# Performance work log

Measured on AMD Instinct MI355X. Metric: run time of the kernel, lower is better.

The kernel has to match this reference:

```python
import jax, jax.numpy as jnp
import numpy as np


def l2norm(t, eps=1e-12):
    # matches F.normalize(p=2, dim=-1): divide by norm clamped to eps
    n = jnp.linalg.norm(t, axis=-1, keepdims=True)
    return t / jnp.maximum(n, eps)


def setup_inputs() -> dict:
    key = jax.random.key(0)
    kx, ke = jax.random.split(key)
    B, N, D, C = 8, 1024, 256, 8192
    x = jax.random.normal(kx, (B, N, D), dtype=jnp.float32)
    # codebook initialized l2-normalized, as in __init__ (kmeans_init=False)
    embed = l2norm(jax.random.normal(ke, (1, C, D), dtype=jnp.float32))
    return {"x": x, "embed": embed}


def reference(x, embed):
    # x: [B, N, D]; ndim < 4 -> add codebook dim h=1
    xh = x[None]                                   # [1, B, N, D]
    h, b, n, d = xh.shape
    flat = l2norm(xh.reshape(h, b * n, d))         # [1, B*N, D]
    e = l2norm(embed)                              # [1, C, D]
    # cosine-similarity distances
    dist = jnp.einsum('hnd,hcd->hnc', flat, e)     # [1, B*N, C]
    # sample_codebook_temp == 0 -> plain argmax
    idx = jnp.argmax(dist, axis=-1).reshape(h, b, n)  # [1, B, N]
    # batched_embedding: gather UN-normalized codebook rows
    quantize = jax.vmap(lambda em, ix: em[ix])(embed, idx)  # [1, B, N, D]
    # needs_codebook_dim -> strip leading dim
    return quantize[0], idx[0]
```

## Files before the change

### kernel.cpp

```cpp
#include <hip/hip_runtime.h>
#include <math.h>

#define QROWS 8192
#define DDIM  256
#define CCNT  8192

typedef __attribute__((ext_vector_type(4))) float f32x4;
typedef __attribute__((ext_vector_type(8))) short bf16x8;

__device__ __forceinline__ unsigned short f2bf(float f) {
    unsigned u = __float_as_uint(f);
    u += 0x7fffu + ((u >> 16) & 1u);
    return (unsigned short)(u >> 16);
}
__device__ __forceinline__ unsigned u32max(unsigned a, unsigned b) { return a > b ? a : b; }
__device__ __forceinline__ unsigned u32min(unsigned a, unsigned b) { return a < b ? a : b; }

__device__ __forceinline__ unsigned key32(float v, unsigned enc) {
    return ((__float_as_uint(v) ^ 0x80000000u) & 0xFFFFFF00u) | enc;
}

__global__ void k_prep(const float* __restrict__ x, unsigned short* __restrict__ xb,
                       const float* __restrict__ e, unsigned short* __restrict__ eb) {
    const int bid = blockIdx.x;
    if (bid < 1024) {
        const int i = (bid * 256 + threadIdx.x) * 8;
        const float4 f0 = *reinterpret_cast<const float4*>(x + i);
        const float4 f1 = *reinterpret_cast<const float4*>(x + i + 4);
        uint4 o;
        o.x = f2bf(f0.x) | ((unsigned)f2bf(f0.y) << 16);
        o.y = f2bf(f0.z) | ((unsigned)f2bf(f0.w) << 16);
        o.z = f2bf(f1.x) | ((unsigned)f2bf(f1.y) << 16);
        o.w = f2bf(f1.z) | ((unsigned)f2bf(f1.w) << 16);
        *reinterpret_cast<uint4*>(xb + i) = o;
    } else {
        const int row  = (bid - 1024) * 4 + (threadIdx.x >> 6);
        const int lane = threadIdx.x & 63;
        const float4 v = *reinterpret_cast<const float4*>(e + (size_t)row * DDIM + lane * 4);
        float s = v.x * v.x + v.y * v.y + v.z * v.z + v.w * v.w;
        #pragma unroll
        for (int off = 1; off < 64; off <<= 1) s += __shfl_xor(s, off);
        const float inv = 1.0f / fmaxf(sqrtf(s), 1e-12f);
        ushort4 o;
        o.x = f2bf(v.x * inv); o.y = f2bf(v.y * inv);
        o.z = f2bf(v.z * inv); o.w = f2bf(v.w * inv);
        *reinterpret_cast<ushort4*>(eb + (size_t)row * DDIM + lane * 4) = o;
    }
}

#define GLOAD_LDS(g, s) \
    __builtin_amdgcn_global_load_lds((const __attribute__((address_space(1))) void*)(g), \
                                     (__attribute__((address_space(3))) void*)(s), 16, 0, 0)

#define SBAR do { asm volatile("" ::: "memory"); __builtin_amdgcn_s_barrier(); \
                  asm volatile("" ::: "memory"); } while (0)
#define WAIT_LGKM(n) do { asm volatile("s_waitcnt lgkmcnt(" #n ")" ::: "memory"); \
                          __builtin_amdgcn_sched_barrier(0); } while (0)
#define WAIT_VM(n) do { asm volatile("s_waitcnt vmcnt(" #n ")" ::: "memory"); \
                        __builtin_amdgcn_sched_barrier(0); } while (0)

__launch_bounds__(512, 2)
__global__ void k_gemm(const unsigned short* __restrict__ xb,
                       const unsigned short* __restrict__ eb,
                       unsigned* pout ) {
    extern __shared__ char smem[];

    const int tid = threadIdx.x;
    const int w = tid >> 6, l = tid & 63;
    const int lg = l >> 4, lr = l & 15, lr7 = lr & 7;
    const int bid = blockIdx.x;
    const int panel = (bid & 7) * 2 + ((bid >> 3) >> 4);
    const int split = (bid >> 3) & 15;
    const int n0 = panel * 512, c0 = split * 512;

    const int lchk = (tid & 24) | ((tid & 7) ^ ((tid >> 5) & 7));
    const char* baseA = (const char*)xb + (size_t)(n0 + (tid >> 5)) * 512 + lchk * 16;
    const char* baseB = (const char*)eb + (size_t)(c0 + (tid >> 5)) * 512 + lchk * 16;
    const int wl16 = w * 1024;

#define STAGE_AHALF(h) do { _Pragma("unroll") for (int g_ = 0; g_ < 16; ++g_)              \
    GLOAD_LDS(baseA + (h) * 131072 + g_ * 8192, smem + g_ * 8192 + wl16); } while (0)
#define STAGEB(t) do { _Pragma("unroll") for (int g_ = 0; g_ < 2; ++g_)                    \
    GLOAD_LDS(baseB + (size_t)(t) * 16384 + g_ * 8192,                                     \
              smem + ((t) & 7) * 16384 + g_ * 8192 + wl16); } while (0)

    bf16x8 aF[4][8];
#define READA() do { _Pragma("unroll") for (int mi_ = 0; mi_ < 4; ++mi_)                   \
    _Pragma("unroll") for (int kk_ = 0; kk_ < 8; ++kk_) {                                  \
        const int lc_ = kk_ * 4 + lg;                                                      \
        const int ph_ = (lc_ & 24) | ((lc_ & 7) ^ lr7);                                    \
        aF[mi_][kk_] = *reinterpret_cast<const bf16x8*>(                                   \
            smem + ((w & 3) * 64 + mi_ * 16 + lr) * 512 + ph_ * 16); } } while (0)

    STAGE_AHALF(0);
    WAIT_VM(0); SBAR;
    if (w < 4) READA();
    WAIT_LGKM(0); SBAR;
    STAGE_AHALF(1);
    WAIT_VM(0); SBAR;
    if (w >= 4) READA();
    WAIT_LGKM(0); SBAR;
    STAGEB(0); STAGEB(1); STAGEB(2); STAGEB(3); STAGEB(4); STAGEB(5);

    const f32x4 zf4 = {0.f, 0.f, 0.f, 0.f};
    unsigned rk1[16], rk2[16];
    #pragma unroll
    for (int i = 0; i < 16; ++i) { rk1[i] = 0u; rk2[i] = 0u; }

#define TILE(t) do {                                                                       \
    const char* sb_ = smem + ((t) & 7) * 16384;                                            \
    f32x4 ac0_[4], ac1_[4];                                                                \
    {                                                                                      \
        const int ph0_ = ((lg & 24) | ((lg & 7) ^ lr7)) * 16;                              \
        const bf16x8 b0_ = *reinterpret_cast<const bf16x8*>(sb_ + lr * 512 + ph0_);        \
        const bf16x8 b1_ = *reinterpret_cast<const bf16x8*>(sb_ + (16 + lr) * 512 + ph0_); \
        _Pragma("unroll") for (int mi_ = 0; mi_ < 4; ++mi_) {                              \
            ac0_[mi_] = __builtin_amdgcn_mfma_f32_16x16x32_bf16(aF[mi_][0], b0_, zf4, 0, 0, 0); \
            ac1_[mi_] = __builtin_amdgcn_mfma_f32_16x16x32_bf16(aF[mi_][0], b1_, zf4, 0, 0, 0); \
        }                                                                                  \
    }                                                                                      \
    _Pragma("unroll") for (int kk_ = 1; kk_ < 8; ++kk_) {                                  \
        const int lc_ = kk_ * 4 + lg;                                                      \
        const int ph_ = ((lc_ & 24) | ((lc_ & 7) ^ lr7)) * 16;                             \
        const bf16x8 b0_ = *reinterpret_cast<const bf16x8*>(sb_ + lr * 512 + ph_);         \
        const bf16x8 b1_ = *reinterpret_cast<const bf16x8*>(sb_ + (16 + lr) * 512 + ph_);  \
        _Pragma("unroll") for (int mi_ = 0; mi_ < 4; ++mi_) {                              \
            ac0_[mi_] = __builtin_amdgcn_mfma_f32_16x16x32_bf16(aF[mi_][kk_], b0_, ac0_[mi_], 0, 0, 0); \
            ac1_[mi_] = __builtin_amdgcn_mfma_f32_16x16x32_bf16(aF[mi_][kk_], b1_, ac1_[mi_], 0, 0, 0); \
        }                                                                                  \
    }                                                                                      \
    const unsigned encb_ = (unsigned)(255 - ((t) & 7) * 32) - (unsigned)lr;                \
    _Pragma("unroll") for (int mi_ = 0; mi_ < 4; ++mi_)                                    \
        _Pragma("unroll") for (int rr_ = 0; rr_ < 4; ++rr_) {                              \
            const unsigned q0_ = key32(ac0_[mi_][rr_], encb_);                             \
            const unsigned q1_ = key32(ac1_[mi_][rr_], encb_ - 16u);                       \
            const unsigned m01_ = u32max(q0_, q1_), n01_ = u32min(q0_, q1_);               \
            const int i_ = mi_ * 4 + rr_;                                                  \
            const unsigned lo_ = u32min(rk1[i_], m01_);                                    \
            rk1[i_] = u32max(rk1[i_], m01_);                                               \
            rk2[i_] = u32max(rk2[i_], u32max(n01_, lo_));                                  \
        }                                                                                  \
} while (0)

#define FLUSH(half) do {                                                                   \
    _Pragma("unroll") for (int i_ = 0; i_ < 16; ++i_) {                                    \
        unsigned t1_ = rk1[i_], t2_ = rk2[i_];                                             \
        _Pragma("unroll") for (int off_ = 1; off_ < 16; off_ <<= 1) {                      \
            const unsigned o1_ = __shfl_xor(t1_, off_);                                    \
            const unsigned o2_ = __shfl_xor(t2_, off_);                                    \
            const unsigned n1_ = u32max(t1_, o1_), lo_ = u32min(t1_, o1_);                 \
            t2_ = u32max(u32max(t2_, o2_), lo_);                                           \
            t1_ = n1_;                                                                     \
        }                                                                                  \
        if (lr == 0) {                                                                     \
            const int row_ = n0 + w * 64 + (i_ >> 2) * 16 + lg * 4 + (i_ & 3);             \
            uint2 o_; o_.x = t1_; o_.y = t2_;                                              \
            *reinterpret_cast<uint2*>(pout + (size_t)row_ * 256 + split * 4 + (half) * 2) = o_; \
        }                                                                                  \
        rk1[i_] = 0u; rk2[i_] = 0u;                                                        \
    }                                                                                      \
} while (0)

    #pragma unroll 1
    for (int u = 0; u < 8; ++u) {
        if (u < 6)       { WAIT_VM(8); }
        else if (u == 6) { WAIT_VM(4); }
        else             { WAIT_VM(0); }
        SBAR;
        if (u < 5) { STAGEB(2 * u + 6); STAGEB(2 * u + 7); }
        TILE(2 * u);
        TILE(2 * u + 1);
        if (u == 3) FLUSH(0);
        if (u == 7) FLUSH(1);
    }
#undef STAGE_AHALF
#undef STAGEB
#undef READA
#undef TILE
#undef FLUSH
}

__global__ void k_fixup(const unsigned* pk,
                        const float* __restrict__ x, const float* __restrict__ e,
                        float* out) {
    const int row = blockIdx.x * 4 + (threadIdx.x >> 6);
    const int t   = threadIdx.x & 63;
    unsigned long long kk0 = 0ull, kk1 = 0ull;
    if (t < 32) {
        const uint2 kv = reinterpret_cast<const uint2*>(pk + (size_t)row * 256)[t];
        const int col0 = t * 256 + 255 - (int)(kv.x & 255u);
        kk0 = ((unsigned long long)(kv.x & 0xFFFFFF00u) << 32) | (unsigned)(~col0);
        const int col1 = t * 256 + 255 - (int)(kv.y & 255u);
        kk1 = ((unsigned long long)(kv.y & 0xFFFFFF00u) << 32) | (unsigned)(~col1);
    }

    int cand[4];
    #pragma unroll
    for (int p = 0; p < 4; ++p) {
        unsigned long long m = kk0 > kk1 ? kk0 : kk1;
        #pragma unroll
        for (int off = 1; off < 64; off <<= 1) {
            const unsigned long long o = __shfl_xor(m, off);
            if (o > m) m = o;
        }
        cand[p] = (int)(~(unsigned)m) & (CCNT - 1);
        if (kk0 == m) kk0 = 0ull;
        if (kk1 == m) kk1 = 0ull;
    }

    const float4 xv = *reinterpret_cast<const float4*>(x + (size_t)row * DDIM + t * 4);
    float best = -INFINITY; int bc = 0x7fffffff;
    #pragma unroll
    for (int p = 0; p < 4; ++p) {
        const int c = cand[p];
        const float4 ev = *reinterpret_cast<const float4*>(e + (size_t)c * DDIM + t * 4);
        float d  = xv.x * ev.x + xv.y * ev.y + xv.z * ev.z + xv.w * ev.w;
        float ss = ev.x * ev.x + ev.y * ev.y + ev.z * ev.z + ev.w * ev.w;
        #pragma unroll
        for (int off = 1; off < 64; off <<= 1) {
            d  += __shfl_xor(d, off);
            ss += __shfl_xor(ss, off);
        }
        const float v = d * (1.0f / fmaxf(sqrtf(ss), 1e-12f));
        if (v > best || (v == best && c < bc)) { best = v; bc = c; }
    }

    if (t == 0) out[(size_t)QROWS * DDIM + row] = (float)bc;
    const float4 q = *reinterpret_cast<const float4*>(e + (size_t)bc * DDIM + t * 4);
    *reinterpret_cast<float4*>(out + (size_t)row * DDIM + t * 4) = q;
}

extern "C" void kernel_launch(void* const* d_in, const int* in_sizes, int n_in,
                              void* d_out, int out_size, void* d_ws, size_t ws_size,
                              hipStream_t stream) {
    const float* x = (const float*)d_in[0];
    const float* e = (const float*)d_in[1];
    float* out = (float*)d_out;
    char* ws = (char*)d_ws;

    unsigned short* xb = (unsigned short*)ws;
    unsigned short* eb = (unsigned short*)(ws + (size_t)4 * 1024 * 1024);

    hipFuncSetAttribute(reinterpret_cast<const void*>(k_gemm),
                        hipFuncAttributeMaxDynamicSharedMemorySize, 131072);

    k_prep<<<3072, 256, 0, stream>>>(x, xb, e, eb);
    k_gemm<<<256, 512, 131072, stream>>>(xb, eb, (unsigned*)d_out);
    k_fixup<<<QROWS / 4, 256, 0, stream>>>((const unsigned*)d_out, x, e, out);
}
```

Measured before the change: 62.46 us.

## Halve GEMM block to 256 threads with 256-row panels and 16-column B tiles

Restructures the fused GEMM+top-2 kernel so each block has 4 waves handling 256 query rows, streams 16-row codebook tiles (twice as many iterations), and launches 512 blocks with 64KB LDS instead of 256 blocks with 128KB. The aim is more resident blocks per CU and better spread of work across the CUs. In exchange, each codebook tile is loaded by twice as many blocks, and each tile does half the MFMA work per B load, which lowers arithmetic intensity. Per-row candidate tracking keeps the same top-2 scheme, now updated with one key per tile instead of two.

```diff
diff --git a/kernel.cpp b/kernel.cpp
--- a/kernel.cpp
+++ b/kernel.cpp
@@ -59,7 +59,7 @@
 #define WAIT_VM(n) do { asm volatile("s_waitcnt vmcnt(" #n ")" ::: "memory"); \
                         __builtin_amdgcn_sched_barrier(0); } while (0)
 
-__launch_bounds__(512, 2)
+__launch_bounds__(256, 2)
 __global__ void k_gemm(const unsigned short* __restrict__ xb,
                        const unsigned short* __restrict__ eb,
                        unsigned* pout ) {
@@ -69,20 +69,21 @@
     const int w = tid >> 6, l = tid & 63;
     const int lg = l >> 4, lr = l & 15, lr7 = lr & 7;
     const int bid = blockIdx.x;
-    const int panel = (bid & 7) * 2 + ((bid >> 3) >> 4);
-    const int split = (bid >> 3) & 15;
-    const int n0 = panel * 512, c0 = split * 512;
+    const int q = bid >> 3;
+    const int panel = (bid & 7) * 4 + (q >> 4);
+    const int split = q & 15;
+    const int n0 = panel * 256, c0 = split * 512;
 
     const int lchk = (tid & 24) | ((tid & 7) ^ ((tid >> 5) & 7));
     const char* baseA = (const char*)xb + (size_t)(n0 + (tid >> 5)) * 512 + lchk * 16;
     const char* baseB = (const char*)eb + (size_t)(c0 + (tid >> 5)) * 512 + lchk * 16;
     const int wl16 = w * 1024;
 
-#define STAGE_AHALF(h) do { _Pragma("unroll") for (int g_ = 0; g_ < 16; ++g_)              \
-    GLOAD_LDS(baseA + (h) * 131072 + g_ * 8192, smem + g_ * 8192 + wl16); } while (0)
+#define STAGE_AROUND(r) do { _Pragma("unroll") for (int g_ = 0; g_ < 16; ++g_)             \
+    GLOAD_LDS(baseA + (r) * 65536 + g_ * 4096, smem + g_ * 4096 + wl16); } while (0)
 #define STAGEB(t) do { _Pragma("unroll") for (int g_ = 0; g_ < 2; ++g_)                    \
-    GLOAD_LDS(baseB + (size_t)(t) * 16384 + g_ * 8192,                                     \
-              smem + ((t) & 7) * 16384 + g_ * 8192 + wl16); } while (0)
+    GLOAD_LDS(baseB + (size_t)(t) * 8192 + g_ * 4096,                                      \
+              smem + ((t) & 7) * 8192 + g_ * 4096 + wl16); } while (0)
 
     bf16x8 aF[4][8];
 #define READA() do { _Pragma("unroll") for (int mi_ = 0; mi_ < 4; ++mi_)                   \
@@ -90,15 +91,15 @@
         const int lc_ = kk_ * 4 + lg;                                                      \
         const int ph_ = (lc_ & 24) | ((lc_ & 7) ^ lr7);                                    \
         aF[mi_][kk_] = *reinterpret_cast<const bf16x8*>(                                   \
-            smem + ((w & 3) * 64 + mi_ * 16 + lr) * 512 + ph_ * 16); } } while (0)
-
-    STAGE_AHALF(0);
+            smem + ((w & 1) * 64 + mi_ * 16 + lr) * 512 + ph_ * 16); } } while (0)
+
+    STAGE_AROUND(0);
     WAIT_VM(0); SBAR;
-    if (w < 4) READA();
+    if (w < 2) READA();
     WAIT_LGKM(0); SBAR;
-    STAGE_AHALF(1);
+    STAGE_AROUND(1);
     WAIT_VM(0); SBAR;
-    if (w >= 4) READA();
+    if (w >= 2) READA();
     WAIT_LGKM(0); SBAR;
     STAGEB(0); STAGEB(1); STAGEB(2); STAGEB(3); STAGEB(4); STAGEB(5);
 
@@ -108,37 +109,29 @@
     for (int i = 0; i < 16; ++i) { rk1[i] = 0u; rk2[i] = 0u; }
 
 #define TILE(t) do {                                                                       \
-    const char* sb_ = smem + ((t) & 7) * 16384;                                            \
-    f32x4 ac0_[4], ac1_[4];                                                                \
+    const char* sb_ = smem + ((t) & 7) * 8192;                                             \
+    f32x4 ac_[4];                                                                          \
     {                                                                                      \
         const int ph0_ = ((lg & 24) | ((lg & 7) ^ lr7)) * 16;                              \
-        const bf16x8 b0_ = *reinterpret_cast<const bf16x8*>(sb_ + lr * 512 + ph0_);        \
-        const bf16x8 b1_ = *reinterpret_cast<const bf16x8*>(sb_ + (16 + lr) * 512 + ph0_); \
-        _Pragma("unroll") for (int mi_ = 0; mi_ < 4; ++mi_) {                              \
-            ac0_[mi_] = __builtin_amdgcn_mfma_f32_16x16x32_bf16(aF[mi_][0], b0_, zf4, 0, 0, 0); \
-            ac1_[mi_] = __builtin_amdgcn_mfma_f32_16x16x32_bf16(aF[mi_][0], b1_, zf4, 0, 0, 0); \
-        }                                                                                  \
+        const bf16x8 b_ = *reinterpret_cast<const bf16x8*>(sb_ + lr * 512 + ph0_);         \
+        _Pragma("unroll") for (int mi_ = 0; mi_ < 4; ++mi_)                                \
+            ac_[mi_] = __builtin_amdgcn_mfma_f32_16x16x32_bf16(aF[mi_][0], b_, zf4, 0, 0, 0); \
     }                                                                                      \
     _Pragma("unroll") for (int kk_ = 1; kk_ < 8; ++kk_) {                                  \
         const int lc_ = kk_ * 4 + lg;                                                      \
         const int ph_ = ((lc_ & 24) | ((lc_ & 7) ^ lr7)) * 16;                             \
-        const bf16x8 b0_ = *reinterpret_cast<const bf16x8*>(sb_ + lr * 512 + ph_);         \
-        const bf16x8 b1_ = *reinterpret_cast<const bf16x8*>(sb_ + (16 + lr) * 512 + ph_);  \
-        _Pragma("unroll") for (int mi_ = 0; mi_ < 4; ++mi_) {                              \
-            ac0_[mi_] = __builtin_amdgcn_mfma_f32_16x16x32_bf16(aF[mi_][kk_], b0_, ac0_[mi_], 0, 0, 0); \
-            ac1_[mi_] = __builtin_amdgcn_mfma_f32_16x16x32_bf16(aF[mi_][kk_], b1_, ac1_[mi_], 0, 0, 0); \
-        }                                                                                  \
+        const bf16x8 b_ = *reinterpret_cast<const bf16x8*>(sb_ + lr * 512 + ph_);          \
+        _Pragma("unroll") for (int mi_ = 0; mi_ < 4; ++mi_)                                \
+            ac_[mi_] = __builtin_amdgcn_mfma_f32_16x16x32_bf16(aF[mi_][kk_], b_, ac_[mi_], 0, 0, 0); \
     }                                                                                      \
-    const unsigned encb_ = (unsigned)(255 - ((t) & 7) * 32) - (unsigned)lr;                \
+    const unsigned encb_ = (unsigned)(255 - ((t) & 15) * 16) - (unsigned)lr;               \
     _Pragma("unroll") for (int mi_ = 0; mi_ < 4; ++mi_)                                    \
         _Pragma("unroll") for (int rr_ = 0; rr_ < 4; ++rr_) {                              \
-            const unsigned q0_ = key32(ac0_[mi_][rr_], encb_);                             \
-            const unsigned q1_ = key32(ac1_[mi_][rr_], encb_ - 16u);                       \
-            const unsigned m01_ = u32max(q0_, q1_), n01_ = u32min(q0_, q1_);               \
+            const unsigned q_ = key32(ac_[mi_][rr_], encb_);                               \
             const int i_ = mi_ * 4 + rr_;                                                  \
-            const unsigned lo_ = u32min(rk1[i_], m01_);                                    \
-            rk1[i_] = u32max(rk1[i_], m01_);                                               \
-            rk2[i_] = u32max(rk2[i_], u32max(n01_, lo_));                                  \
+            const unsigned lo_ = u32min(rk1[i_], q_);                                      \
+            rk1[i_] = u32max(rk1[i_], q_);                                                 \
+            rk2[i_] = u32max(rk2[i_], lo_);                                                \
         }                                                                                  \
 } while (0)
 
@@ -162,18 +155,18 @@
 } while (0)
 
     #pragma unroll 1
-    for (int u = 0; u < 8; ++u) {
-        if (u < 6)       { WAIT_VM(8); }
-        else if (u == 6) { WAIT_VM(4); }
+    for (int u = 0; u < 16; ++u) {
+        if (u < 14)      { WAIT_VM(8); }
+        else if (u == 14){ WAIT_VM(4); }
         else             { WAIT_VM(0); }
         SBAR;
-        if (u < 5) { STAGEB(2 * u + 6); STAGEB(2 * u + 7); }
+        if (u < 13) { STAGEB(2 * u + 6); STAGEB(2 * u + 7); }
         TILE(2 * u);
         TILE(2 * u + 1);
-        if (u == 3) FLUSH(0);
-        if (u == 7) FLUSH(1);
-    }
-#undef STAGE_AHALF
+        if (u == 7)  FLUSH(0);
+        if (u == 15) FLUSH(1);
+    }
+#undef STAGE_AROUND
 #undef STAGEB
 #undef READA
 #undef TILE
@@ -226,8 +219,8 @@
     }
 
     if (t == 0) out[(size_t)QROWS * DDIM + row] = (float)bc;
-    const float4 q = *reinterpret_cast<const float4*>(e + (size_t)bc * DDIM + t * 4);
-    *reinterpret_cast<float4*>(out + (size_t)row * DDIM + t * 4) = q;
+    const float4 qv = *reinterpret_cast<const float4*>(e + (size_t)bc * DDIM + t * 4);
+    *reinterpret_cast<float4*>(out + (size_t)row * DDIM + t * 4) = qv;
 }
 
 extern "C" void kernel_launch(void* const* d_in, const int* in_sizes, int n_in,
@@ -242,9 +235,9 @@
     unsigned short* eb = (unsigned short*)(ws + (size_t)4 * 1024 * 1024);
 
     hipFuncSetAttribute(reinterpret_cast<const void*>(k_gemm),
-                        hipFuncAttributeMaxDynamicSharedMemorySize, 131072);
+                        hipFuncAttributeMaxDynamicSharedMemorySize, 65536);
 
     k_prep<<<3072, 256, 0, stream>>>(x, xb, e, eb);
-    k_gemm<<<256, 512, 131072, stream>>>(xb, eb, (unsigned*)d_out);
+    k_gemm<<<512, 256, 65536, stream>>>(xb, eb, (unsigned*)d_out);
     k_fixup<<<QROWS / 4, 256, 0, stream>>>((const unsigned*)d_out, x, e, out);
 }
```

Result: faster. 61.09 us (-2.2%).
